# Kernel tuning notes

Measured on AMD Instinct MI355X. Metric: run time of the kernel, lower is better.

## Reference

```python
import jax, jax.numpy as jnp
import numpy as np

PI = float(np.pi)


def _layernorm(x, g, b, eps=1e-5):
    mu = jnp.mean(x, axis=-1, keepdims=True)
    var = jnp.var(x, axis=-1, keepdims=True)
    return (x - mu) * jax.lax.rsqrt(var + eps) * g + b


def setup_inputs() -> dict:
    key = jax.random.key(0)
    B, L, D, P = 4, 2048, 256, 32
    ks = jax.random.split(key, 16)

    def lin_w(k, fi, fo):
        return (jax.random.normal(k, (fi, fo), dtype=jnp.float32) / np.sqrt(fi)).astype(jnp.float32)

    inp = {
        'x': jax.random.normal(ks[0], (B, L, D), dtype=jnp.float32),
        'pos_phases': jax.random.normal(ks[1], (L, P), dtype=jnp.float32) * PI,
        'w_mem1v': lin_w(ks[2], D, P), 'b_mem1v': jnp.zeros((P,), jnp.float32),
        'w_mem1o': lin_w(ks[3], P, D), 'b_mem1o': jnp.zeros((D,), jnp.float32),
        'w_off': lin_w(ks[4], D + P, P), 'b_off': jnp.zeros((P,), jnp.float32),
        'w_key': lin_w(ks[5], D, P), 'b_key': jnp.zeros((P,), jnp.float32),
        'w_val': lin_w(ks[6], D, D), 'b_val': jnp.zeros((D,), jnp.float32),
        'w_sk1': lin_w(ks[7], 2 * D, D), 'b_sk1': jnp.zeros((D,), jnp.float32),
        'w_sk2': lin_w(ks[8], D, P), 'b_sk2': jnp.zeros((P,), jnp.float32),
        'w_gate': lin_w(ks[9], D, 1), 'b_gate': jnp.zeros((1,), jnp.float32),
        'ln_g': jnp.ones((D,), jnp.float32), 'ln_b': jnp.zeros((D,), jnp.float32),
        'w_out': lin_w(ks[10], D, D), 'b_out': jnp.zeros((D,), jnp.float32),
    }
    return inp


def reference(x, pos_phases, w_mem1v, b_mem1v, w_mem1o, b_mem1o, w_off, b_off,
              w_key, b_key, w_val, b_val, w_sk1, b_sk1, w_sk2, b_sk2,
              w_gate, b_gate, ln_g, ln_b, w_out, b_out):
    B, L, D = x.shape
    P = pos_phases.shape[-1]

    pos_cos = jnp.cos(pos_phases)  # [L,P]
    pos_sin = jnp.sin(pos_phases)

    # Memory 1: flat [B,L,P] phasor cumulative memory
    v1 = x @ w_mem1v + b_mem1v                       # [B,L,P]
    mem1_cos = jnp.cumsum(pos_cos[None] * v1, axis=1)
    mem1_sin = jnp.cumsum(pos_sin[None] * v1, axis=1)

    offset_input = jnp.concatenate([x, jnp.broadcast_to(pos_phases[None], (B, L, P))], axis=-1)
    offset = jnp.tanh(offset_input @ w_off + b_off) * PI
    oc, os = jnp.cos(offset), jnp.sin(offset)
    query_cos = pos_cos[None] * oc - pos_sin[None] * os
    query_sin = pos_sin[None] * oc + pos_cos[None] * os
    pos_ret = (mem1_cos * query_cos + mem1_sin * query_sin) / np.sqrt(P)
    pos_out = pos_ret @ w_mem1o + b_mem1o            # [B,L,D]

    # Memory 2: full [B,L,P,D] phasor KV cumulative memory
    key_phases = jnp.tanh(x @ w_key + b_key) * PI    # [B,L,P]
    key_cos, key_sin = jnp.cos(key_phases), jnp.sin(key_phases)
    values = x @ w_val + b_val                       # [B,L,D]
    store_gate = jax.nn.sigmoid(x @ w_gate + b_gate) # [B,L,1]

    positions = jnp.arange(1, L + 1, dtype=x.dtype)[None, :, None]
    context_avg = jnp.cumsum(x, axis=1) / positions
    h = jax.nn.gelu(jnp.concatenate([x, context_avg], axis=-1) @ w_sk1 + b_sk1, approximate=False)
    storage_phases = jnp.tanh(h @ w_sk2 + b_sk2) * PI  # [B,L,P]

    gated_v = values * store_gate                    # [B,L,D]
    kv_mem_cos = jnp.cumsum(jnp.cos(storage_phases)[..., None] * gated_v[:, :, None, :], axis=1)  # [B,L,P,D]
    kv_mem_sin = jnp.cumsum(jnp.sin(storage_phases)[..., None] * gated_v[:, :, None, :], axis=1)

    gate_cumsum = jnp.clip(jnp.cumsum(store_gate, axis=1), 1.0, None)  # [B,L,1]
    kv_retrieved = jnp.einsum('blpd,blp->bld', kv_mem_cos, key_cos) + \
                   jnp.einsum('blpd,blp->bld', kv_mem_sin, key_sin)
    kv_retrieved = kv_retrieved / (jnp.sqrt(gate_cumsum) * np.sqrt(P))

    combined = pos_out + kv_retrieved
    return x + _layernorm(combined, ln_g, ln_b) @ w_out + b_out
```

## Files before the change

kernel.cpp:

```cpp
#include <hip/hip_runtime.h>
#include <hip/hip_bf16.h>

constexpr int B_ = 4;
constexpr int L_ = 2048;
constexpr int D_ = 256;
constexpr int P_ = 32;
constexpr int CL = 32;
constexpr int NC = L_ / CL;

#define PI_F 3.14159265358979323846f
#define INV_SQRT_P 0.17677669529663687f

typedef __attribute__((ext_vector_type(8))) short short8_t;
typedef __attribute__((ext_vector_type(4))) float floatx4;

static __device__ inline short f2bf(float f) {
  unsigned int u;
  __builtin_memcpy(&u, &f, 4);
  unsigned int r = (u + 0x7fffu + ((u >> 16) & 1u)) >> 16;
  return (short)r;
}
static __device__ inline float bf2f(short s) {
  unsigned int u = ((unsigned int)(unsigned short)s) << 16;
  float f;
  __builtin_memcpy(&f, &u, 4);
  return f;
}

__global__ void wprep(const float* __restrict__ x, const float* __restrict__ pos,
                      const float* __restrict__ w_val, const float* __restrict__ w_mem1v,
                      const float* __restrict__ w_off, const float* __restrict__ b_off,
                      const float* __restrict__ w_key, const float* __restrict__ w_gate,
                      const float* __restrict__ w_sk1, const float* __restrict__ w_out,
                      const float* __restrict__ w_sk2, const float* __restrict__ w_mem1o,
                      short* __restrict__ WA, short* __restrict__ W1,
                      short* __restrict__ WO, short* __restrict__ W2T,
                      short* __restrict__ W1OT,
                      short* __restrict__ xbf, float* __restrict__ poff,
                      float* __restrict__ ctxsum) {
  int blk = blockIdx.x, tid = threadIdx.x;
  if (blk < 384) {
    int idx = blk * 256 + tid;
    int n = idx >> 8, k = idx & 255;
    float v;
    if (n < 256) v = w_val[k * 256 + n];
    else if (n < 288) v = w_mem1v[k * 32 + (n - 256)];
    else if (n < 320) v = w_off[k * 32 + (n - 288)];
    else if (n < 352) v = w_key[k * 32 + (n - 320)];
    else if (n == 352) v = w_gate[k];
    else v = 0.f;
    WA[idx] = f2bf(v);
  } else if (blk < 896) {
    int idx = (blk - 384) * 256 + tid;
    int n = idx >> 9, k = idx & 511;
    W1[idx] = f2bf(w_sk1[k * 256 + n]);
  } else if (blk < 1152) {
    int idx = (blk - 896) * 256 + tid;
    int n = idx >> 8, k = idx & 255;
    WO[idx] = f2bf(w_out[k * 256 + n]);
  } else if (blk < 1184) {
    int idx = (blk - 1152) * 256 + tid;
    int p = idx >> 8, k = idx & 255;
    W2T[idx] = f2bf(w_sk2[k * 32 + p]);
  } else if (blk < 1216) {
    int idx = (blk - 1184) * 256 + tid;
    int d = idx >> 5, p = idx & 31;
    W1OT[idx] = f2bf(w_mem1o[p * 256 + d]);
  } else if (blk < 3264) {
    int idx = ((blk - 1216) * 256 + tid) * 4;
    float4 v = *(const float4*)&x[idx];
    short4 o;
    o.x = f2bf(v.x); o.y = f2bf(v.y); o.z = f2bf(v.z); o.w = f2bf(v.w);
    *(short4*)&xbf[idx] = o;
  } else if (blk < 3520) {
    int idx = (blk - 3264) * 256 + tid;
    int l = idx >> 5, p = idx & 31;
    float a = b_off[p];
#pragma unroll 8
    for (int j = 0; j < 32; ++j) a += pos[l * 32 + j] * w_off[(256 + j) * 32 + p];
    poff[idx] = a;
  } else {
    int c2 = blk - 3520;
    int b = c2 >> 6, ch = c2 & 63;
    int xb = (b * L_ + ch * 32) * 256 + tid;
    float s = 0.f;
#pragma unroll 8
    for (int i = 0; i < 32; ++i) s += x[xb + i * 256];
    ctxsum[c2 * 256 + tid] = s;
  }
}

template <int KTILES, int MODE>
__global__ __launch_bounds__(256, 4) void gemm32(const short* __restrict__ A0,
                                                 const short* __restrict__ A1,
                                                 const short* __restrict__ W,
                                                 const float* __restrict__ bias,
                                                 const float* __restrict__ xres,
                                                 float* __restrict__ outf,
                                                 short* __restrict__ outb) {
  __shared__ short As[32][136];
  __shared__ short Bs[64][136];
  int tid = threadIdx.x;
  int mg = blockIdx.x >> 2, ng = blockIdx.x & 3;
  int tok0 = mg * 32, n0 = ng * 64;
  int lane = tid & 63, w = tid >> 6;
  int nw = w * 16;
  floatx4 acc[2] = {{0.f, 0.f, 0.f, 0.f}, {0.f, 0.f, 0.f, 0.f}};
  int r2 = tid >> 4, c8 = tid & 15;
  int ml = lane & 15, quad = lane >> 4, kq = quad * 8;
  const int K = KTILES * 128;

  for (int kt = 0; kt < KTILES; ++kt) {
    const short* Asrc;
    int cb;
    if (KTILES == 4) {
      Asrc = (kt < 2) ? A0 : A1;
      cb = (kt & 1) * 128;
    } else {
      Asrc = A0;
      cb = kt * 128;
    }
#pragma unroll
    for (int pass = 0; pass < 2; ++pass) {
      int row = pass * 16 + r2;
      *(short8_t*)&As[row][c8 * 8] =
          *(const short8_t*)&Asrc[(tok0 + row) * 256 + cb + c8 * 8];
    }
#pragma unroll
    for (int pass = 0; pass < 4; ++pass) {
      int row = pass * 16 + r2;
      *(short8_t*)&Bs[row][c8 * 8] =
          *(const short8_t*)&W[(n0 + row) * K + kt * 128 + c8 * 8];
    }
    __syncthreads();
#pragma unroll
    for (int s = 0; s < 4; ++s) {
      short8_t a0 = *(short8_t*)&As[ml][s * 32 + kq];
      short8_t a1 = *(short8_t*)&As[16 + ml][s * 32 + kq];
      short8_t b0 = *(short8_t*)&Bs[nw + ml][s * 32 + kq];
      acc[0] = __builtin_amdgcn_mfma_f32_16x16x32_bf16(a0, b0, acc[0], 0, 0, 0);
      acc[1] = __builtin_amdgcn_mfma_f32_16x16x32_bf16(a1, b0, acc[1], 0, 0, 0);
    }
    __syncthreads();
  }
  int n = n0 + nw + ml;
  float bv = bias ? bias[n] : 0.f;
#pragma unroll
  for (int mt = 0; mt < 2; ++mt) {
#pragma unroll
    for (int rg = 0; rg < 4; ++rg) {
      int tok = tok0 + mt * 16 + quad * 4 + rg;
      float v = acc[mt][rg] + bv;
      if (MODE == 1) {
        float g = 0.5f * v * (1.f + erff(v * 0.70710678118654752f));
        outb[tok * 256 + n] = f2bf(g);
      } else {
        outf[tok * 256 + n] = xres[tok * 256 + n] + v;
      }
    }
  }
}

__global__ __launch_bounds__(384, 3) void gemmA3(const short* __restrict__ xbf,
                                                 const short* __restrict__ WA,
                                                 const float* __restrict__ pos,
                                                 const float* __restrict__ poff,
                                                 const float* __restrict__ b_mem1v,
                                                 const float* __restrict__ b_key,
                                                 const float* __restrict__ b_gate,
                                                 const float* __restrict__ b_val,
                                                 float* __restrict__ m1cT,
                                                 float* __restrict__ m1sT,
                                                 float* __restrict__ qc,
                                                 float* __restrict__ qs,
                                                 short* __restrict__ K2bf,
                                                 short* __restrict__ gvT,
                                                 float* __restrict__ sg) {
  __shared__ float YL[16][132];
  __shared__ float gsh[16];
  int tid = threadIdx.x;
  int lane = tid & 63, w = tid >> 6;
  int ml = lane & 15, quad = lane >> 4, kq = quad * 8;
  int bc = blockIdx.x;
  int bc32 = bc >> 1, half = bc & 1;
  int tok0 = bc * 16;
  floatx4 acc[4] = {};
  const short* A0p = &xbf[(tok0 + ml) * 256 + kq];
  const short* Bp = &WA[(w * 64 + ml) * 256 + kq];
#pragma unroll
  for (int ks = 0; ks < 8; ++ks) {
    short8_t a0 = *(const short8_t*)(A0p + ks * 32);
#pragma unroll
    for (int nt = 0; nt < 4; ++nt) {
      short8_t b = *(const short8_t*)(Bp + nt * 16 * 256 + ks * 32);
      acc[nt] = __builtin_amdgcn_mfma_f32_16x16x32_bf16(a0, b, acc[nt], 0, 0, 0);
    }
  }
  if (w >= 4) {
#pragma unroll
    for (int nt = 0; nt < 4; ++nt) {
      int col = (w - 4) * 64 + nt * 16 + ml;
#pragma unroll
      for (int r = 0; r < 4; ++r)
        YL[quad * 4 + r][col] = acc[nt][r];
    }
  }
  __syncthreads();
  if (tid < 256) {
#pragma unroll
    for (int it = 0; it < 2; ++it) {
      int idx = it * 256 + tid;
      int t = idx >> 5, p = idx & 31;
      int tok = tok0 + t, l = tok & (L_ - 1);
      int b = tok >> 11;
      float v1 = YL[t][p] + b_mem1v[p];
      float ph = pos[l * 32 + p];
      float pc = cosf(ph), ps = sinf(ph);
      int idxT = (b * 32 + p) * L_ + l;
      m1cT[idxT] = pc * v1;
      m1sT[idxT] = ps * v1;
      float off = tanhf(YL[t][32 + p] + poff[l * 32 + p]) * PI_F;
      float oc = cosf(off), os = sinf(off);
      int gidx = tok * 32 + p;
      qc[gidx] = pc * oc - ps * os;
      qs[gidx] = ps * oc + pc * os;
      float kp = tanhf(YL[t][64 + p] + b_key[p]) * PI_F;
      K2bf[tok * 64 + p] = f2bf(cosf(kp));
      K2bf[tok * 64 + 32 + p] = f2bf(sinf(kp));
      if (p == 0) {
        float g = 1.f / (1.f + expf(-(YL[t][96] + b_gate[0])));
        sg[tok] = g;
        gsh[t] = g;
      }
    }
  }
  __syncthreads();
  if (w < 4) {
#pragma unroll
    for (int nt = 0; nt < 4; ++nt) {
      int d = w * 64 + nt * 16 + ml;
      float bv = b_val[d];
      int t0 = quad * 4;
      short4 o;
      o.x = f2bf((acc[nt][0] + bv) * gsh[t0 + 0]);
      o.y = f2bf((acc[nt][1] + bv) * gsh[t0 + 1]);
      o.z = f2bf((acc[nt][2] + bv) * gsh[t0 + 2]);
      o.w = f2bf((acc[nt][3] + bv) * gsh[t0 + 3]);
      *(short4*)&gvT[(bc32 * 256 + d) * 32 + half * 16 + t0] = o;
    }
  }
}

__global__ void scan_all(float* __restrict__ m1cT, float* __restrict__ m1sT,
                         float* __restrict__ sg, const float* __restrict__ x,
                         const float* __restrict__ ctxsum, short* __restrict__ ctxbf) {
  int blk = blockIdx.x;
  int tid = threadIdx.x;
  if (blk >= 260) {
    int c2 = blk - 260;
    int b = c2 >> 6, ch = c2 & 63;
    float run = 0.f;
    int sb = b * 64 * 256 + tid;
    int c = 0;
    for (; c + 8 <= ch; c += 8) {
      float t0 = ctxsum[sb + (c + 0) * 256];
      float t1 = ctxsum[sb + (c + 1) * 256];
      float t2 = ctxsum[sb + (c + 2) * 256];
      float t3 = ctxsum[sb + (c + 3) * 256];
      float t4 = ctxsum[sb + (c + 4) * 256];
      float t5 = ctxsum[sb + (c + 5) * 256];
      float t6 = ctxsum[sb + (c + 6) * 256];
      float t7 = ctxsum[sb + (c + 7) * 256];
      run += ((t0 + t1) + (t2 + t3)) + ((t4 + t5) + (t6 + t7));
    }
    for (; c < ch; ++c) run += ctxsum[sb + c * 256];
    int xb = (b * L_ + ch * 32) * 256 + tid;
#pragma unroll 8
    for (int i = 0; i < 32; ++i) {
      run += x[xb + i * 256];
      int l = ch * 32 + i;
      ctxbf[xb + i * 256] = f2bf(run / (float)(l + 1));
    }
    return;
  }
  int lane = tid & 63, wid = tid >> 6;
  __shared__ float wsum[4];
  float carry = 0.f;
  float* arr;
  int base;
  if (blk < 256) {
    arr = (blk < 128) ? m1cT : m1sT;
    base = (blk & 127) * L_;
  } else {
    arr = sg;
    base = (blk - 256) * L_;
  }
  float v[8];
#pragma unroll
  for (int i = 0; i < 8; ++i) v[i] = arr[base + i * 256 + tid];
#pragma unroll
  for (int i = 0; i < 8; ++i) {
    float vv = v[i];
#pragma unroll
    for (int off = 1; off < 64; off <<= 1) {
      float n = __shfl_up(vv, off, 64);
      if (lane >= off) vv += n;
    }
    if (lane == 63) wsum[wid] = vv;
    __syncthreads();
    float add = carry;
    for (int w = 0; w < wid; ++w) add += wsum[w];
    arr[base + i * 256 + tid] = vv + add;
    carry += wsum[0] + wsum[1] + wsum[2] + wsum[3];
    __syncthreads();
  }
}

__global__ __launch_bounds__(256, 2) void kernelCD(const short* __restrict__ hs,
                                                   const short* __restrict__ W2T,
                                                   const float* __restrict__ b_sk2,
                                                   const short* __restrict__ gvT,
                                                   short* __restrict__ SPbf,
                                                   short* __restrict__ UT) {
  __shared__ __align__(16) short SPL[64][40];
  int tid = threadIdx.x;
  int bc = blockIdx.x >> 1, dh = blockIdx.x & 1;
  int tok0 = bc * 32;
  int lane = tid & 63, w = tid >> 6;
  int ml = lane & 15, quad = lane >> 4, kq = quad * 8;
  int th = w & 1, ph = w >> 1;
  floatx4 pacc = {};
#pragma unroll
  for (int s = 0; s < 8; ++s) {
    short8_t a = *(const short8_t*)&hs[(tok0 + th * 16 + ml) * 256 + s * 32 + kq];
    short8_t b0 = *(const short8_t*)&W2T[(ph * 16 + ml) * 256 + s * 32 + kq];
    pacc = __builtin_amdgcn_mfma_f32_16x16x32_bf16(a, b0, pacc, 0, 0, 0);
  }
  {
    int p = ph * 16 + ml;
    float bs = b_sk2[p];
#pragma unroll
    for (int r = 0; r < 4; ++r) {
      int tl = th * 16 + quad * 4 + r;
      int tok = tok0 + tl;
      float sp = tanhf(pacc[r] + bs) * PI_F;
      short c = f2bf(cosf(sp)), s = f2bf(sinf(sp));
      SPL[p][tl] = c;
      SPL[32 + p][tl] = s;
      if (dh == 0) {
        SPbf[tok * 64 + p] = c;
        SPbf[tok * 64 + 32 + p] = s;
      }
    }
  }
  __syncthreads();
  short8_t a[4];
#pragma unroll
  for (int mt = 0; mt < 4; ++mt) a[mt] = *(short8_t*)&SPL[mt * 16 + ml][kq];
  floatx4 acc[4][2] = {};
#pragma unroll
  for (int nt = 0; nt < 2; ++nt) {
    int d = dh * 128 + w * 32 + nt * 16 + ml;
    short8_t b = *(const short8_t*)&gvT[(bc * 256 + d) * 32 + kq];
#pragma unroll
    for (int mt = 0; mt < 4; ++mt)
      acc[mt][nt] = __builtin_amdgcn_mfma_f32_16x16x32_bf16(a[mt], b, acc[mt][nt], 0, 0, 0);
  }
#pragma unroll
  for (int mt = 0; mt < 4; ++mt)
#pragma unroll
    for (int nt = 0; nt < 2; ++nt) {
      int d = dh * 128 + w * 32 + nt * 16 + ml;
      short4 o;
      o.x = f2bf(acc[mt][nt][0]);
      o.y = f2bf(acc[mt][nt][1]);
      o.z = f2bf(acc[mt][nt][2]);
      o.w = f2bf(acc[mt][nt][3]);
      *(short4*)&UT[(bc * 256 + d) * 64 + mt * 16 + quad * 4] = o;
    }
}

__global__ void kernelE(short* __restrict__ UT) {
  int tid = blockIdx.x * 256 + threadIdx.x;
  int q = tid & 63;
  int d = (tid >> 6) & 255;
  int b = tid >> 14;
  int base = ((b * NC) * 256 + d) * 64 + q;
  const int cs = 256 * 64;
  short v[64];
#pragma unroll
  for (int c = 0; c < 64; ++c) v[c] = UT[base + c * cs];
  float run = 0.f;
#pragma unroll
  for (int c = 0; c < 64; ++c) {
    UT[base + c * cs] = f2bf(run);
    run += bf2f(v[c]);
  }
}

__global__ __launch_bounds__(512, 2) void kernelFG(const short* __restrict__ UT,
                                                   const short* __restrict__ SPbf,
                                                   const short* __restrict__ K2bf,
                                                   const short* __restrict__ gvT,
                                                   const float* __restrict__ sgc,
                                                   const float* __restrict__ m1cT,
                                                   const float* __restrict__ m1sT,
                                                   const float* __restrict__ qc,
                                                   const float* __restrict__ qs,
                                                   const short* __restrict__ W1OT,
                                                   const float* __restrict__ b_mem1o,
                                                   const float* __restrict__ ln_g,
                                                   const float* __restrict__ ln_b,
                                                   short* __restrict__ cbn) {
  __shared__ __align__(16) short SL[32][40];
  __shared__ __align__(16) short PR[32][40];
  __shared__ float CMB[32][260];
  __shared__ float scl[32], mu_s[32], rs_s[32];
  int tid = threadIdx.x;
  int bc = blockIdx.x;
  int lbase = bc * CL;
  int bb = bc >> 6, lloc = (bc & 63) * 32;
  if (tid < 32) scl[tid] = rsqrtf(fmaxf(sgc[lbase + tid], 1.f)) * INV_SQRT_P;
#pragma unroll
  for (int it = 0; it < 2; ++it) {
    int i = it * 512 + tid;
    int p = i >> 5, t = i & 31;
    int gT = (bb * 32 + p) * L_ + lloc + t;
    int g = (lbase + t) * 32 + p;
    PR[t][p] = f2bf((m1cT[gT] * qc[g] + m1sT[gT] * qs[g]) * INV_SQRT_P);
  }
  int lane = tid & 63, w = tid >> 6;
  int ml = lane & 15, quad = lane >> 4, kq = quad * 8;
  int d0 = w * 32;
  floatx4 acc[2][2] = {};
  short8_t ka0 = *(const short8_t*)&K2bf[(lbase + ml) * 64 + kq];
  short8_t ka1 = *(const short8_t*)&K2bf[(lbase + 16 + ml) * 64 + kq];
  short8_t kb0 = *(const short8_t*)&K2bf[(lbase + ml) * 64 + 32 + kq];
  short8_t kb1 = *(const short8_t*)&K2bf[(lbase + 16 + ml) * 64 + 32 + kq];
#pragma unroll
  for (int nt = 0; nt < 2; ++nt) {
    short8_t b = *(const short8_t*)&UT[(bc * 256 + d0 + nt * 16 + ml) * 64 + kq];
    acc[0][nt] = __builtin_amdgcn_mfma_f32_16x16x32_bf16(ka0, b, acc[0][nt], 0, 0, 0);
    acc[1][nt] = __builtin_amdgcn_mfma_f32_16x16x32_bf16(ka1, b, acc[1][nt], 0, 0, 0);
  }
  if (w == 0) {
    floatx4 sacc[2][2] = {};
#pragma unroll
    for (int ks2 = 0; ks2 < 2; ++ks2) {
      short8_t a0 = (ks2 == 0) ? ka0 : kb0;
      short8_t a1 = (ks2 == 0) ? ka1 : kb1;
      short8_t b0 = *(const short8_t*)&SPbf[(lbase + ml) * 64 + ks2 * 32 + kq];
      short8_t b1 = *(const short8_t*)&SPbf[(lbase + 16 + ml) * 64 + ks2 * 32 + kq];
      sacc[0][0] = __builtin_amdgcn_mfma_f32_16x16x32_bf16(a0, b0, sacc[0][0], 0, 0, 0);
      sacc[0][1] = __builtin_amdgcn_mfma_f32_16x16x32_bf16(a0, b1, sacc[0][1], 0, 0, 0);
      sacc[1][0] = __builtin_amdgcn_mfma_f32_16x16x32_bf16(a1, b0, sacc[1][0], 0, 0, 0);
      sacc[1][1] = __builtin_amdgcn_mfma_f32_16x16x32_bf16(a1, b1, sacc[1][1], 0, 0, 0);
    }
#pragma unroll
    for (int mt = 0; mt < 2; ++mt)
#pragma unroll
      for (int nt = 0; nt < 2; ++nt)
#pragma unroll
        for (int r = 0; r < 4; ++r) {
          int trow = mt * 16 + quad * 4 + r;
          int scol = nt * 16 + ml;
          float v = (scol <= trow) ? sacc[mt][nt][r] : 0.f;
          SL[trow][scol] = f2bf(v);
        }
  }
  __syncthreads();
#pragma unroll
  for (int nt = 0; nt < 2; ++nt) {
    short8_t b = *(const short8_t*)&UT[(bc * 256 + d0 + nt * 16 + ml) * 64 + 32 + kq];
    acc[0][nt] = __builtin_amdgcn_mfma_f32_16x16x32_bf16(kb0, b, acc[0][nt], 0, 0, 0);
    acc[1][nt] = __builtin_amdgcn_mfma_f32_16x16x32_bf16(kb1, b, acc[1][nt], 0, 0, 0);
  }
  {
    short8_t a0 = *(short8_t*)&SL[ml][kq];
    short8_t a1 = *(short8_t*)&SL[16 + ml][kq];
#pragma unroll
    for (int nt = 0; nt < 2; ++nt) {
      short8_t b = *(const short8_t*)&gvT[(bc * 256 + d0 + nt * 16 + ml) * 32 + kq];
      acc[0][nt] = __builtin_amdgcn_mfma_f32_16x16x32_bf16(a0, b, acc[0][nt], 0, 0, 0);
      acc[1][nt] = __builtin_amdgcn_mfma_f32_16x16x32_bf16(a1, b, acc[1][nt], 0, 0, 0);
    }
  }
  floatx4 macc[2][2] = {};
  {
    short8_t a0 = *(short8_t*)&PR[ml][kq];
    short8_t a1 = *(short8_t*)&PR[16 + ml][kq];
#pragma unroll
    for (int nt = 0; nt < 2; ++nt) {
      short8_t b = *(const short8_t*)&W1OT[(d0 + nt * 16 + ml) * 32 + kq];
      macc[0][nt] = __builtin_amdgcn_mfma_f32_16x16x32_bf16(a0, b, macc[0][nt], 0, 0, 0);
      macc[1][nt] = __builtin_amdgcn_mfma_f32_16x16x32_bf16(a1, b, macc[1][nt], 0, 0, 0);
    }
  }
#pragma unroll
  for (int mt = 0; mt < 2; ++mt)
#pragma unroll
    for (int nt = 0; nt < 2; ++nt) {
      int d = d0 + nt * 16 + ml;
      float bm = b_mem1o[d];
#pragma unroll
      for (int r = 0; r < 4; ++r) {
        int t = mt * 16 + quad * 4 + r;
        CMB[t][d] = acc[mt][nt][r] * scl[t] + macc[mt][nt][r] + bm;
      }
    }
  __syncthreads();
  {
    int t = tid >> 4, g = tid & 15;
    float s = 0.f, s2 = 0.f;
#pragma unroll
    for (int j = 0; j < 16; ++j) {
      float v = CMB[t][g + j * 16];
      s += v;
      s2 += v * v;
    }
#pragma unroll
    for (int m = 1; m < 16; m <<= 1) {
      s += __shfl_xor(s, m, 64);
      s2 += __shfl_xor(s2, m, 64);
    }
    if (g == 0) {
      float mu = s / (float)D_;
      float var = s2 / (float)D_ - mu * mu;
      mu_s[t] = mu;
      rs_s[t] = rsqrtf(var + 1e-5f);
    }
  }
  __syncthreads();
  {
    int d = tid & 255, th = tid >> 8;
    float lg = ln_g[d], lb = ln_b[d];
#pragma unroll
    for (int i = 0; i < 16; ++i) {
      int t = th * 16 + i;
      cbn[(lbase + t) * 256 + d] = f2bf((CMB[t][d] - mu_s[t]) * rs_s[t] * lg + lb);
    }
  }
}

extern "C" void kernel_launch(void* const* d_in, const int* in_sizes, int n_in,
                              void* d_out, int out_size, void* d_ws, size_t ws_size,
                              hipStream_t stream) {
  const float* x = (const float*)d_in[0];
  const float* pos = (const float*)d_in[1];
  const float* w_mem1v = (const float*)d_in[2];
  const float* b_mem1v = (const float*)d_in[3];
  const float* w_mem1o = (const float*)d_in[4];
  const float* b_mem1o = (const float*)d_in[5];
  const float* w_off = (const float*)d_in[6];
  const float* b_off = (const float*)d_in[7];
  const float* w_key = (const float*)d_in[8];
  const float* b_key = (const float*)d_in[9];
  const float* w_val = (const float*)d_in[10];
  const float* b_val = (const float*)d_in[11];
  const float* w_sk1 = (const float*)d_in[12];
  const float* b_sk1 = (const float*)d_in[13];
  const float* w_sk2 = (const float*)d_in[14];
  const float* b_sk2 = (const float*)d_in[15];
  const float* w_gate = (const float*)d_in[16];
  const float* b_gate = (const float*)d_in[17];
  const float* ln_g = (const float*)d_in[18];
  const float* ln_b = (const float*)d_in[19];
  const float* w_out = (const float*)d_in[20];
  const float* b_out = (const float*)d_in[21];
  float* out = (float*)d_out;
  float* ws = (float*)d_ws;

  const int BLP = B_ * L_ * P_;
  const int BLD = B_ * L_ * D_;
  float* m1cT = ws;
  float* m1sT = m1cT + BLP;
  float* qc = m1sT + BLP;
  float* qs = qc + BLP;
  float* sg = qs + BLP;
  float* poff = sg + B_ * L_;
  float* ctxsum = poff + L_ * P_;
  short* UT = (short*)(ctxsum + B_ * 64 * 256);
  short* xbf = UT + (size_t)B_ * NC * 256 * 64;
  short* cbn = xbf;
  short* ctxbf = xbf + BLD;
  short* hs = ctxbf + BLD;
  short* gvT = hs + BLD;
  short* K2bf = gvT + BLD;
  short* SPbf = K2bf + B_ * L_ * 64;
  short* WA = SPbf + B_ * L_ * 64;
  short* W1 = WA + 384 * 256;
  short* WO = W1 + 256 * 512;
  short* W2T = WO + 256 * 256;
  short* W1OT = W2T + 32 * 256;

  wprep<<<3776, 256, 0, stream>>>(x, pos, w_val, w_mem1v, w_off, b_off, w_key, w_gate,
                                  w_sk1, w_out, w_sk2, w_mem1o, WA, W1, WO, W2T, W1OT,
                                  xbf, poff, ctxsum);
  gemmA3<<<512, 384, 0, stream>>>(xbf, WA, pos, poff, b_mem1v, b_key, b_gate, b_val,
                                  m1cT, m1sT, qc, qs, K2bf, gvT, sg);
  scan_all<<<516, 256, 0, stream>>>(m1cT, m1sT, sg, x, ctxsum, ctxbf);
  gemm32<4, 1><<<256 * 4, 256, 0, stream>>>(xbf, ctxbf, W1, b_sk1, nullptr, nullptr, hs);
  kernelCD<<<512, 256, 0, stream>>>(hs, W2T, b_sk2, gvT, SPbf, UT);
  kernelE<<<256, 256, 0, stream>>>(UT);
  kernelFG<<<B_ * NC, 512, 0, stream>>>(UT, SPbf, K2bf, gvT, sg, m1cT, m1sT, qc, qs,
                                        W1OT, b_mem1o, ln_g, ln_b, cbn);
  gemm32<2, 2><<<256 * 4, 256, 0, stream>>>(cbn, nullptr, WO, b_out, x, out, nullptr);
}
```

Before: 171.5 us.

## Merge all stages into one cooperative persistent kernel with grid syncs

```diff
diff --git a/kernel.cpp b/kernel.cpp
--- a/kernel.cpp
+++ b/kernel.cpp
@@ -1,5 +1,8 @@
 #include <hip/hip_runtime.h>
 #include <hip/hip_bf16.h>
+#include <hip/hip_cooperative_groups.h>
+
+namespace cg = cooperative_groups;
 
 constexpr int B_ = 4;
 constexpr int L_ = 2048;
@@ -27,519 +30,521 @@
   return f;
 }
 
-__global__ void wprep(const float* __restrict__ x, const float* __restrict__ pos,
-                      const float* __restrict__ w_val, const float* __restrict__ w_mem1v,
-                      const float* __restrict__ w_off, const float* __restrict__ b_off,
-                      const float* __restrict__ w_key, const float* __restrict__ w_gate,
-                      const float* __restrict__ w_sk1, const float* __restrict__ w_out,
-                      const float* __restrict__ w_sk2, const float* __restrict__ w_mem1o,
-                      short* __restrict__ WA, short* __restrict__ W1,
-                      short* __restrict__ WO, short* __restrict__ W2T,
-                      short* __restrict__ W1OT,
-                      short* __restrict__ xbf, float* __restrict__ poff,
-                      float* __restrict__ ctxsum) {
-  int blk = blockIdx.x, tid = threadIdx.x;
-  if (blk < 384) {
-    int idx = blk * 256 + tid;
-    int n = idx >> 8, k = idx & 255;
-    float v;
-    if (n < 256) v = w_val[k * 256 + n];
-    else if (n < 288) v = w_mem1v[k * 32 + (n - 256)];
-    else if (n < 320) v = w_off[k * 32 + (n - 288)];
-    else if (n < 352) v = w_key[k * 32 + (n - 320)];
-    else if (n == 352) v = w_gate[k];
-    else v = 0.f;
-    WA[idx] = f2bf(v);
-  } else if (blk < 896) {
-    int idx = (blk - 384) * 256 + tid;
-    int n = idx >> 9, k = idx & 511;
-    W1[idx] = f2bf(w_sk1[k * 256 + n]);
-  } else if (blk < 1152) {
-    int idx = (blk - 896) * 256 + tid;
-    int n = idx >> 8, k = idx & 255;
-    WO[idx] = f2bf(w_out[k * 256 + n]);
-  } else if (blk < 1184) {
-    int idx = (blk - 1152) * 256 + tid;
-    int p = idx >> 8, k = idx & 255;
-    W2T[idx] = f2bf(w_sk2[k * 32 + p]);
-  } else if (blk < 1216) {
-    int idx = (blk - 1184) * 256 + tid;
-    int d = idx >> 5, p = idx & 31;
-    W1OT[idx] = f2bf(w_mem1o[p * 256 + d]);
-  } else if (blk < 3264) {
-    int idx = ((blk - 1216) * 256 + tid) * 4;
-    float4 v = *(const float4*)&x[idx];
-    short4 o;
-    o.x = f2bf(v.x); o.y = f2bf(v.y); o.z = f2bf(v.z); o.w = f2bf(v.w);
-    *(short4*)&xbf[idx] = o;
-  } else if (blk < 3520) {
-    int idx = (blk - 3264) * 256 + tid;
-    int l = idx >> 5, p = idx & 31;
-    float a = b_off[p];
-#pragma unroll 8
-    for (int j = 0; j < 32; ++j) a += pos[l * 32 + j] * w_off[(256 + j) * 32 + p];
-    poff[idx] = a;
-  } else {
-    int c2 = blk - 3520;
-    int b = c2 >> 6, ch = c2 & 63;
-    int xb = (b * L_ + ch * 32) * 256 + tid;
-    float s = 0.f;
-#pragma unroll 8
-    for (int i = 0; i < 32; ++i) s += x[xb + i * 256];
-    ctxsum[c2 * 256 + tid] = s;
-  }
-}
+union __align__(16) SMem {
+  struct { float YL[2][16][132]; float gsh[2][16]; } a3;
+  struct { short As[2][32][136]; short Bs[2][64][136]; } g32;
+  struct { short SPL[2][64][40]; } cd;
+  struct { short SL[32][40]; short PR[32][40]; float CMB[32][260];
+           float scl[32]; float mu_s[32]; float rs_s[32]; } fg;
+};
 
 template <int KTILES, int MODE>
-__global__ __launch_bounds__(256, 4) void gemm32(const short* __restrict__ A0,
-                                                 const short* __restrict__ A1,
-                                                 const short* __restrict__ W,
-                                                 const float* __restrict__ bias,
-                                                 const float* __restrict__ xres,
-                                                 float* __restrict__ outf,
-                                                 short* __restrict__ outb) {
-  __shared__ short As[32][136];
-  __shared__ short Bs[64][136];
-  int tid = threadIdx.x;
-  int mg = blockIdx.x >> 2, ng = blockIdx.x & 3;
-  int tok0 = mg * 32, n0 = ng * 64;
+__device__ __forceinline__ void phase_gemm(const short* __restrict__ A0,
+                                           const short* __restrict__ A1,
+                                           const short* __restrict__ W,
+                                           const float* __restrict__ bias,
+                                           const float* __restrict__ xres,
+                                           float* __restrict__ outf,
+                                           short* __restrict__ outb,
+                                           SMem* sm, int bid, int tid5) {
+  int sub = tid5 >> 8, tid = tid5 & 255;
   int lane = tid & 63, w = tid >> 6;
   int nw = w * 16;
-  floatx4 acc[2] = {{0.f, 0.f, 0.f, 0.f}, {0.f, 0.f, 0.f, 0.f}};
   int r2 = tid >> 4, c8 = tid & 15;
   int ml = lane & 15, quad = lane >> 4, kq = quad * 8;
   const int K = KTILES * 128;
-
-  for (int kt = 0; kt < KTILES; ++kt) {
-    const short* Asrc;
-    int cb;
-    if (KTILES == 4) {
-      Asrc = (kt < 2) ? A0 : A1;
-      cb = (kt & 1) * 128;
+  for (int pass = 0; pass < 2; ++pass) {
+    int vb = pass * 512 + bid * 2 + sub;
+    int mg = vb >> 2, ng = vb & 3;
+    int tok0 = mg * 32, n0 = ng * 64;
+    floatx4 acc[2] = {{0.f, 0.f, 0.f, 0.f}, {0.f, 0.f, 0.f, 0.f}};
+    for (int kt = 0; kt < KTILES; ++kt) {
+      const short* Asrc;
+      int cb;
+      if (KTILES == 4) {
+        Asrc = (kt < 2) ? A0 : A1;
+        cb = (kt & 1) * 128;
+      } else {
+        Asrc = A0;
+        cb = kt * 128;
+      }
+#pragma unroll
+      for (int p2 = 0; p2 < 2; ++p2) {
+        int row = p2 * 16 + r2;
+        *(short8_t*)&sm->g32.As[sub][row][c8 * 8] =
+            *(const short8_t*)&Asrc[(tok0 + row) * 256 + cb + c8 * 8];
+      }
+#pragma unroll
+      for (int p2 = 0; p2 < 4; ++p2) {
+        int row = p2 * 16 + r2;
+        *(short8_t*)&sm->g32.Bs[sub][row][c8 * 8] =
+            *(const short8_t*)&W[(n0 + row) * K + kt * 128 + c8 * 8];
+      }
+      __syncthreads();
+#pragma unroll
+      for (int s = 0; s < 4; ++s) {
+        short8_t a0 = *(short8_t*)&sm->g32.As[sub][ml][s * 32 + kq];
+        short8_t a1 = *(short8_t*)&sm->g32.As[sub][16 + ml][s * 32 + kq];
+        short8_t b0 = *(short8_t*)&sm->g32.Bs[sub][nw + ml][s * 32 + kq];
+        acc[0] = __builtin_amdgcn_mfma_f32_16x16x32_bf16(a0, b0, acc[0], 0, 0, 0);
+        acc[1] = __builtin_amdgcn_mfma_f32_16x16x32_bf16(a1, b0, acc[1], 0, 0, 0);
+      }
+      __syncthreads();
+    }
+    int n = n0 + nw + ml;
+    float bv = bias[n];
+#pragma unroll
+    for (int mt = 0; mt < 2; ++mt) {
+#pragma unroll
+      for (int rg = 0; rg < 4; ++rg) {
+        int tok = tok0 + mt * 16 + quad * 4 + rg;
+        float v = acc[mt][rg] + bv;
+        if (MODE == 1) {
+          float g = 0.5f * v * (1.f + erff(v * 0.70710678118654752f));
+          outb[tok * 256 + n] = f2bf(g);
+        } else {
+          outf[tok * 256 + n] = xres[tok * 256 + n] + v;
+        }
+      }
+    }
+  }
+}
+
+__global__ __launch_bounds__(512, 2) void mega(
+    const float* __restrict__ x, const float* __restrict__ pos,
+    const float* __restrict__ w_val, const float* __restrict__ w_mem1v,
+    const float* __restrict__ w_off, const float* __restrict__ b_off,
+    const float* __restrict__ w_key, const float* __restrict__ w_gate,
+    const float* __restrict__ w_sk1, const float* __restrict__ w_out,
+    const float* __restrict__ w_sk2, const float* __restrict__ w_mem1o,
+    const float* __restrict__ b_mem1v, const float* __restrict__ b_key,
+    const float* __restrict__ b_gate, const float* __restrict__ b_val,
+    const float* __restrict__ b_sk1, const float* __restrict__ b_sk2,
+    const float* __restrict__ b_mem1o, const float* __restrict__ ln_g,
+    const float* __restrict__ ln_b, const float* __restrict__ b_out,
+    float* __restrict__ out, float* __restrict__ ws) {
+  __shared__ SMem sm;
+  cg::grid_group grid = cg::this_grid();
+  int bid = blockIdx.x;
+  int tid5 = threadIdx.x;
+  int sub = tid5 >> 8, tid = tid5 & 255;
+
+  const int BLP = B_ * L_ * P_;
+  const int BLD = B_ * L_ * D_;
+  float* m1cT = ws;
+  float* m1sT = m1cT + BLP;
+  float* qc = m1sT + BLP;
+  float* qs = qc + BLP;
+  float* sg = qs + BLP;
+  float* poff = sg + B_ * L_;
+  float* ctxsum = poff + L_ * P_;
+  short* UT = (short*)(ctxsum + B_ * 64 * 256);
+  short* xbf = UT + (size_t)B_ * NC * 256 * 64;
+  short* cbn = xbf;
+  short* ctxbf = xbf + BLD;
+  short* hs = ctxbf + BLD;
+  short* gvT = hs + BLD;
+  short* K2bf = gvT + BLD;
+  short* SPbf = K2bf + B_ * L_ * 64;
+  short* WA = SPbf + B_ * L_ * 64;
+  short* W1 = WA + 384 * 256;
+  short* WO = W1 + 256 * 512;
+  short* W2T = WO + 256 * 256;
+  short* W1OT = W2T + 32 * 256;
+
+  for (int p = 0; p < 8; ++p) {
+    int blk = p * 512 + bid * 2 + sub;
+    if (blk >= 3776) break;
+    if (blk < 384) {
+      int idx = blk * 256 + tid;
+      int n = idx >> 8, k = idx & 255;
+      float v;
+      if (n < 256) v = w_val[k * 256 + n];
+      else if (n < 288) v = w_mem1v[k * 32 + (n - 256)];
+      else if (n < 320) v = w_off[k * 32 + (n - 288)];
+      else if (n < 352) v = w_key[k * 32 + (n - 320)];
+      else if (n == 352) v = w_gate[k];
+      else v = 0.f;
+      WA[idx] = f2bf(v);
+    } else if (blk < 896) {
+      int idx = (blk - 384) * 256 + tid;
+      int n = idx >> 9, k = idx & 511;
+      W1[idx] = f2bf(w_sk1[k * 256 + n]);
+    } else if (blk < 1152) {
+      int idx = (blk - 896) * 256 + tid;
+      int n = idx >> 8, k = idx & 255;
+      WO[idx] = f2bf(w_out[k * 256 + n]);
+    } else if (blk < 1184) {
+      int idx = (blk - 1152) * 256 + tid;
+      int pp = idx >> 8, k = idx & 255;
+      W2T[idx] = f2bf(w_sk2[k * 32 + pp]);
+    } else if (blk < 1216) {
+      int idx = (blk - 1184) * 256 + tid;
+      int d = idx >> 5, pp = idx & 31;
+      W1OT[idx] = f2bf(w_mem1o[pp * 256 + d]);
+    } else if (blk < 3264) {
+      int idx = ((blk - 1216) * 256 + tid) * 4;
+      float4 v = *(const float4*)&x[idx];
+      short4 o;
+      o.x = f2bf(v.x); o.y = f2bf(v.y); o.z = f2bf(v.z); o.w = f2bf(v.w);
+      *(short4*)&xbf[idx] = o;
+    } else if (blk < 3520) {
+      int idx = (blk - 3264) * 256 + tid;
+      int l = idx >> 5, pp = idx & 31;
+      float a = b_off[pp];
+#pragma unroll 8
+      for (int j = 0; j < 32; ++j) a += pos[l * 32 + j] * w_off[(256 + j) * 32 + pp];
+      poff[idx] = a;
     } else {
-      Asrc = A0;
-      cb = kt * 128;
-    }
-#pragma unroll
-    for (int pass = 0; pass < 2; ++pass) {
-      int row = pass * 16 + r2;
-      *(short8_t*)&As[row][c8 * 8] =
-          *(const short8_t*)&Asrc[(tok0 + row) * 256 + cb + c8 * 8];
-    }
-#pragma unroll
-    for (int pass = 0; pass < 4; ++pass) {
-      int row = pass * 16 + r2;
-      *(short8_t*)&Bs[row][c8 * 8] =
-          *(const short8_t*)&W[(n0 + row) * K + kt * 128 + c8 * 8];
+      int c2 = blk - 3520;
+      int b = c2 >> 6, ch = c2 & 63;
+      int xb = (b * L_ + ch * 32) * 256 + tid;
+      float s = 0.f;
+#pragma unroll 8
+      for (int i = 0; i < 32; ++i) s += x[xb + i * 256];
+      ctxsum[c2 * 256 + tid] = s;
+    }
+  }
+  grid.sync();
+
+  {
+    int lane = tid & 63, w = tid >> 6;
+    int ml = lane & 15, quad = lane >> 4, kq = quad * 8;
+    int vb = bid * 2 + sub;
+    int bc32 = vb >> 1, half = vb & 1;
+    int tok0 = vb * 16;
+    floatx4 acc[6] = {};
+    const short* A0p = &xbf[(tok0 + ml) * 256 + kq];
+    const short* Bp = &WA[(w * 96 + ml) * 256 + kq];
+#pragma unroll
+    for (int ks = 0; ks < 8; ++ks) {
+      short8_t a0 = *(const short8_t*)(A0p + ks * 32);
+#pragma unroll
+      for (int nt = 0; nt < 6; ++nt) {
+        short8_t b = *(const short8_t*)(Bp + nt * 16 * 256 + ks * 32);
+        acc[nt] = __builtin_amdgcn_mfma_f32_16x16x32_bf16(a0, b, acc[nt], 0, 0, 0);
+      }
+    }
+#pragma unroll
+    for (int nt = 0; nt < 6; ++nt) {
+      int col = w * 96 + nt * 16 + ml;
+      if (col >= 256) {
+#pragma unroll
+        for (int r = 0; r < 4; ++r) sm.a3.YL[sub][quad * 4 + r][col - 256] = acc[nt][r];
+      }
     }
     __syncthreads();
-#pragma unroll
-    for (int s = 0; s < 4; ++s) {
-      short8_t a0 = *(short8_t*)&As[ml][s * 32 + kq];
-      short8_t a1 = *(short8_t*)&As[16 + ml][s * 32 + kq];
-      short8_t b0 = *(short8_t*)&Bs[nw + ml][s * 32 + kq];
-      acc[0] = __builtin_amdgcn_mfma_f32_16x16x32_bf16(a0, b0, acc[0], 0, 0, 0);
-      acc[1] = __builtin_amdgcn_mfma_f32_16x16x32_bf16(a1, b0, acc[1], 0, 0, 0);
-    }
-    __syncthreads();
-  }
-  int n = n0 + nw + ml;
-  float bv = bias ? bias[n] : 0.f;
-#pragma unroll
-  for (int mt = 0; mt < 2; ++mt) {
-#pragma unroll
-    for (int rg = 0; rg < 4; ++rg) {
-      int tok = tok0 + mt * 16 + quad * 4 + rg;
-      float v = acc[mt][rg] + bv;
-      if (MODE == 1) {
-        float g = 0.5f * v * (1.f + erff(v * 0.70710678118654752f));
-        outb[tok * 256 + n] = f2bf(g);
-      } else {
-        outf[tok * 256 + n] = xres[tok * 256 + n] + v;
-      }
-    }
-  }
-}
-
-__global__ __launch_bounds__(384, 3) void gemmA3(const short* __restrict__ xbf,
-                                                 const short* __restrict__ WA,
-                                                 const float* __restrict__ pos,
-                                                 const float* __restrict__ poff,
-                                                 const float* __restrict__ b_mem1v,
-                                                 const float* __restrict__ b_key,
-                                                 const float* __restrict__ b_gate,
-                                                 const float* __restrict__ b_val,
-                                                 float* __restrict__ m1cT,
-                                                 float* __restrict__ m1sT,
-                                                 float* __restrict__ qc,
-                                                 float* __restrict__ qs,
-                                                 short* __restrict__ K2bf,
-                                                 short* __restrict__ gvT,
-                                                 float* __restrict__ sg) {
-  __shared__ float YL[16][132];
-  __shared__ float gsh[16];
-  int tid = threadIdx.x;
-  int lane = tid & 63, w = tid >> 6;
-  int ml = lane & 15, quad = lane >> 4, kq = quad * 8;
-  int bc = blockIdx.x;
-  int bc32 = bc >> 1, half = bc & 1;
-  int tok0 = bc * 16;
-  floatx4 acc[4] = {};
-  const short* A0p = &xbf[(tok0 + ml) * 256 + kq];
-  const short* Bp = &WA[(w * 64 + ml) * 256 + kq];
-#pragma unroll
-  for (int ks = 0; ks < 8; ++ks) {
-    short8_t a0 = *(const short8_t*)(A0p + ks * 32);
-#pragma unroll
-    for (int nt = 0; nt < 4; ++nt) {
-      short8_t b = *(const short8_t*)(Bp + nt * 16 * 256 + ks * 32);
-      acc[nt] = __builtin_amdgcn_mfma_f32_16x16x32_bf16(a0, b, acc[nt], 0, 0, 0);
-    }
-  }
-  if (w >= 4) {
-#pragma unroll
-    for (int nt = 0; nt < 4; ++nt) {
-      int col = (w - 4) * 64 + nt * 16 + ml;
-#pragma unroll
-      for (int r = 0; r < 4; ++r)
-        YL[quad * 4 + r][col] = acc[nt][r];
-    }
-  }
-  __syncthreads();
-  if (tid < 256) {
 #pragma unroll
     for (int it = 0; it < 2; ++it) {
       int idx = it * 256 + tid;
-      int t = idx >> 5, p = idx & 31;
+      int t = idx >> 5, pp = idx & 31;
       int tok = tok0 + t, l = tok & (L_ - 1);
       int b = tok >> 11;
-      float v1 = YL[t][p] + b_mem1v[p];
-      float ph = pos[l * 32 + p];
+      float v1 = sm.a3.YL[sub][t][pp] + b_mem1v[pp];
+      float ph = pos[l * 32 + pp];
       float pc = cosf(ph), ps = sinf(ph);
-      int idxT = (b * 32 + p) * L_ + l;
+      int idxT = (b * 32 + pp) * L_ + l;
       m1cT[idxT] = pc * v1;
       m1sT[idxT] = ps * v1;
-      float off = tanhf(YL[t][32 + p] + poff[l * 32 + p]) * PI_F;
+      float off = tanhf(sm.a3.YL[sub][t][32 + pp] + poff[l * 32 + pp]) * PI_F;
       float oc = cosf(off), os = sinf(off);
-      int gidx = tok * 32 + p;
+      int gidx = tok * 32 + pp;
       qc[gidx] = pc * oc - ps * os;
       qs[gidx] = ps * oc + pc * os;
-      float kp = tanhf(YL[t][64 + p] + b_key[p]) * PI_F;
-      K2bf[tok * 64 + p] = f2bf(cosf(kp));
-      K2bf[tok * 64 + 32 + p] = f2bf(sinf(kp));
-      if (p == 0) {
-        float g = 1.f / (1.f + expf(-(YL[t][96] + b_gate[0])));
+      float kp = tanhf(sm.a3.YL[sub][t][64 + pp] + b_key[pp]) * PI_F;
+      K2bf[tok * 64 + pp] = f2bf(cosf(kp));
+      K2bf[tok * 64 + 32 + pp] = f2bf(sinf(kp));
+      if (pp == 0) {
+        float g = 1.f / (1.f + expf(-(sm.a3.YL[sub][t][96] + b_gate[0])));
         sg[tok] = g;
-        gsh[t] = g;
-      }
-    }
-  }
-  __syncthreads();
-  if (w < 4) {
-#pragma unroll
-    for (int nt = 0; nt < 4; ++nt) {
-      int d = w * 64 + nt * 16 + ml;
-      float bv = b_val[d];
-      int t0 = quad * 4;
-      short4 o;
-      o.x = f2bf((acc[nt][0] + bv) * gsh[t0 + 0]);
-      o.y = f2bf((acc[nt][1] + bv) * gsh[t0 + 1]);
-      o.z = f2bf((acc[nt][2] + bv) * gsh[t0 + 2]);
-      o.w = f2bf((acc[nt][3] + bv) * gsh[t0 + 3]);
-      *(short4*)&gvT[(bc32 * 256 + d) * 32 + half * 16 + t0] = o;
-    }
-  }
-}
-
-__global__ void scan_all(float* __restrict__ m1cT, float* __restrict__ m1sT,
-                         float* __restrict__ sg, const float* __restrict__ x,
-                         const float* __restrict__ ctxsum, short* __restrict__ ctxbf) {
-  int blk = blockIdx.x;
-  int tid = threadIdx.x;
-  if (blk >= 260) {
-    int c2 = blk - 260;
-    int b = c2 >> 6, ch = c2 & 63;
-    float run = 0.f;
-    int sb = b * 64 * 256 + tid;
-    int c = 0;
-    for (; c + 8 <= ch; c += 8) {
-      float t0 = ctxsum[sb + (c + 0) * 256];
-      float t1 = ctxsum[sb + (c + 1) * 256];
-      float t2 = ctxsum[sb + (c + 2) * 256];
-      float t3 = ctxsum[sb + (c + 3) * 256];
-      float t4 = ctxsum[sb + (c + 4) * 256];
-      float t5 = ctxsum[sb + (c + 5) * 256];
-      float t6 = ctxsum[sb + (c + 6) * 256];
-      float t7 = ctxsum[sb + (c + 7) * 256];
-      run += ((t0 + t1) + (t2 + t3)) + ((t4 + t5) + (t6 + t7));
-    }
-    for (; c < ch; ++c) run += ctxsum[sb + c * 256];
-    int xb = (b * L_ + ch * 32) * 256 + tid;
+        sm.a3.gsh[sub][t] = g;
+      }
+    }
+    __syncthreads();
+#pragma unroll
+    for (int nt = 0; nt < 6; ++nt) {
+      int col = w * 96 + nt * 16 + ml;
+      if (col < 256) {
+        float bv = b_val[col];
+        int t0 = quad * 4;
+        short4 o;
+        o.x = f2bf((acc[nt][0] + bv) * sm.a3.gsh[sub][t0 + 0]);
+        o.y = f2bf((acc[nt][1] + bv) * sm.a3.gsh[sub][t0 + 1]);
+        o.z = f2bf((acc[nt][2] + bv) * sm.a3.gsh[sub][t0 + 2]);
+        o.w = f2bf((acc[nt][3] + bv) * sm.a3.gsh[sub][t0 + 3]);
+        *(short4*)&gvT[(bc32 * 256 + col) * 32 + half * 16 + t0] = o;
+      }
+    }
+  }
+  grid.sync();
+
+  {
+    int gw = bid * 8 + (tid5 >> 6);
+    int lane = tid5 & 63;
+    if (gw < 260) {
+      float* arr;
+      int base;
+      if (gw < 128) { arr = m1cT; base = gw * L_; }
+      else if (gw < 256) { arr = m1sT; base = (gw - 128) * L_; }
+      else { arr = sg; base = (gw - 256) * L_; }
+      float v[32];
+#pragma unroll
+      for (int i = 0; i < 32; ++i) v[i] = arr[base + i * 64 + lane];
+      float carry = 0.f;
+#pragma unroll
+      for (int i = 0; i < 32; ++i) {
+        float vv = v[i];
+#pragma unroll
+        for (int off = 1; off < 64; off <<= 1) {
+          float n = __shfl_up(vv, off, 64);
+          if (lane >= off) vv += n;
+        }
+        vv += carry;
+        arr[base + i * 64 + lane] = vv;
+        carry = __shfl(vv, 63, 64);
+      }
+    } else if (gw >= 1024) {
+      int ct = gw - 1024;
+      int c2 = ct >> 2, dp = ct & 3;
+      int b = c2 >> 6, ch = c2 & 63;
+      int d = dp * 64 + lane;
+      float run = 0.f;
+      int sb = b * 64 * 256 + d;
+      int c = 0;
+      for (; c + 8 <= ch; c += 8) {
+        float t0 = ctxsum[sb + (c + 0) * 256];
+        float t1 = ctxsum[sb + (c + 1) * 256];
+        float t2 = ctxsum[sb + (c + 2) * 256];
+        float t3 = ctxsum[sb + (c + 3) * 256];
+        float t4 = ctxsum[sb + (c + 4) * 256];
+        float t5 = ctxsum[sb + (c + 5) * 256];
+        float t6 = ctxsum[sb + (c + 6) * 256];
+        float t7 = ctxsum[sb + (c + 7) * 256];
+        run += ((t0 + t1) + (t2 + t3)) + ((t4 + t5) + (t6 + t7));
+      }
+      for (; c < ch; ++c) run += ctxsum[sb + c * 256];
+      int xb = (b * L_ + ch * 32) * 256 + d;
 #pragma unroll 8
-    for (int i = 0; i < 32; ++i) {
-      run += x[xb + i * 256];
-      int l = ch * 32 + i;
-      ctxbf[xb + i * 256] = f2bf(run / (float)(l + 1));
-    }
-    return;
-  }
-  int lane = tid & 63, wid = tid >> 6;
-  __shared__ float wsum[4];
-  float carry = 0.f;
-  float* arr;
-  int base;
-  if (blk < 256) {
-    arr = (blk < 128) ? m1cT : m1sT;
-    base = (blk & 127) * L_;
-  } else {
-    arr = sg;
-    base = (blk - 256) * L_;
-  }
-  float v[8];
-#pragma unroll
-  for (int i = 0; i < 8; ++i) v[i] = arr[base + i * 256 + tid];
-#pragma unroll
-  for (int i = 0; i < 8; ++i) {
-    float vv = v[i];
-#pragma unroll
-    for (int off = 1; off < 64; off <<= 1) {
-      float n = __shfl_up(vv, off, 64);
-      if (lane >= off) vv += n;
-    }
-    if (lane == 63) wsum[wid] = vv;
+      for (int i = 0; i < 32; ++i) {
+        run += x[xb + i * 256];
+        int l = ch * 32 + i;
+        ctxbf[xb + i * 256] = f2bf(run / (float)(l + 1));
+      }
+    }
+  }
+  grid.sync();
+
+  phase_gemm<4, 1>(xbf, ctxbf, W1, b_sk1, nullptr, nullptr, hs, &sm, bid, tid5);
+  grid.sync();
+
+  {
+    int lane = tid & 63, w = tid >> 6;
+    int ml = lane & 15, quad = lane >> 4, kq = quad * 8;
+    int vb = bid * 2 + sub;
+    int bc = vb >> 1, dh = vb & 1;
+    int tok0 = bc * 32;
+    int th = w & 1, ph = w >> 1;
+    floatx4 pacc = {};
+#pragma unroll
+    for (int s = 0; s < 8; ++s) {
+      short8_t a = *(const short8_t*)&hs[(tok0 + th * 16 + ml) * 256 + s * 32 + kq];
+      short8_t b0 = *(const short8_t*)&W2T[(ph * 16 + ml) * 256 + s * 32 + kq];
+      pacc = __builtin_amdgcn_mfma_f32_16x16x32_bf16(a, b0, pacc, 0, 0, 0);
+    }
+    {
+      int pp = ph * 16 + ml;
+      float bs = b_sk2[pp];
+#pragma unroll
+      for (int r = 0; r < 4; ++r) {
+        int tl = th * 16 + quad * 4 + r;
+        int tok = tok0 + tl;
+        float sp = tanhf(pacc[r] + bs) * PI_F;
+        short c = f2bf(cosf(sp)), s2 = f2bf(sinf(sp));
+        sm.cd.SPL[sub][pp][tl] = c;
+        sm.cd.SPL[sub][32 + pp][tl] = s2;
+        if (dh == 0) {
+          SPbf[tok * 64 + pp] = c;
+          SPbf[tok * 64 + 32 + pp] = s2;
+        }
+      }
+    }
     __syncthreads();
-    float add = carry;
-    for (int w = 0; w < wid; ++w) add += wsum[w];
-    arr[base + i * 256 + tid] = vv + add;
-    carry += wsum[0] + wsum[1] + wsum[2] + wsum[3];
-    __syncthreads();
-  }
-}
-
-__global__ __launch_bounds__(256, 2) void kernelCD(const short* __restrict__ hs,
-                                                   const short* __restrict__ W2T,
-                                                   const float* __restrict__ b_sk2,
-                                                   const short* __restrict__ gvT,
-                                                   short* __restrict__ SPbf,
-                                                   short* __restrict__ UT) {
-  __shared__ __align__(16) short SPL[64][40];
-  int tid = threadIdx.x;
-  int bc = blockIdx.x >> 1, dh = blockIdx.x & 1;
-  int tok0 = bc * 32;
-  int lane = tid & 63, w = tid >> 6;
-  int ml = lane & 15, quad = lane >> 4, kq = quad * 8;
-  int th = w & 1, ph = w >> 1;
-  floatx4 pacc = {};
-#pragma unroll
-  for (int s = 0; s < 8; ++s) {
-    short8_t a = *(const short8_t*)&hs[(tok0 + th * 16 + ml) * 256 + s * 32 + kq];
-    short8_t b0 = *(const short8_t*)&W2T[(ph * 16 + ml) * 256 + s * 32 + kq];
-    pacc = __builtin_amdgcn_mfma_f32_16x16x32_bf16(a, b0, pacc, 0, 0, 0);
-  }
-  {
-    int p = ph * 16 + ml;
-    float bs = b_sk2[p];
-#pragma unroll
-    for (int r = 0; r < 4; ++r) {
-      int tl = th * 16 + quad * 4 + r;
-      int tok = tok0 + tl;
-      float sp = tanhf(pacc[r] + bs) * PI_F;
-      short c = f2bf(cosf(sp)), s = f2bf(sinf(sp));
-      SPL[p][tl] = c;
-      SPL[32 + p][tl] = s;
-      if (dh == 0) {
-        SPbf[tok * 64 + p] = c;
-        SPbf[tok * 64 + 32 + p] = s;
-      }
-    }
-  }
-  __syncthreads();
-  short8_t a[4];
-#pragma unroll
-  for (int mt = 0; mt < 4; ++mt) a[mt] = *(short8_t*)&SPL[mt * 16 + ml][kq];
-  floatx4 acc[4][2] = {};
-#pragma unroll
-  for (int nt = 0; nt < 2; ++nt) {
-    int d = dh * 128 + w * 32 + nt * 16 + ml;
-    short8_t b = *(const short8_t*)&gvT[(bc * 256 + d) * 32 + kq];
-#pragma unroll
-    for (int mt = 0; mt < 4; ++mt)
-      acc[mt][nt] = __builtin_amdgcn_mfma_f32_16x16x32_bf16(a[mt], b, acc[mt][nt], 0, 0, 0);
-  }
-#pragma unroll
-  for (int mt = 0; mt < 4; ++mt)
+    short8_t a[4];
+#pragma unroll
+    for (int mt = 0; mt < 4; ++mt) a[mt] = *(short8_t*)&sm.cd.SPL[sub][mt * 16 + ml][kq];
+    floatx4 acc[4][2] = {};
 #pragma unroll
     for (int nt = 0; nt < 2; ++nt) {
       int d = dh * 128 + w * 32 + nt * 16 + ml;
-      short4 o;
-      o.x = f2bf(acc[mt][nt][0]);
-      o.y = f2bf(acc[mt][nt][1]);
-      o.z = f2bf(acc[mt][nt][2]);
-      o.w = f2bf(acc[mt][nt][3]);
-      *(short4*)&UT[(bc * 256 + d) * 64 + mt * 16 + quad * 4] = o;
-    }
-}
-
-__global__ void kernelE(short* __restrict__ UT) {
-  int tid = blockIdx.x * 256 + threadIdx.x;
-  int q = tid & 63;
-  int d = (tid >> 6) & 255;
-  int b = tid >> 14;
-  int base = ((b * NC) * 256 + d) * 64 + q;
-  const int cs = 256 * 64;
-  short v[64];
-#pragma unroll
-  for (int c = 0; c < 64; ++c) v[c] = UT[base + c * cs];
-  float run = 0.f;
-#pragma unroll
-  for (int c = 0; c < 64; ++c) {
-    UT[base + c * cs] = f2bf(run);
-    run += bf2f(v[c]);
-  }
-}
-
-__global__ __launch_bounds__(512, 2) void kernelFG(const short* __restrict__ UT,
-                                                   const short* __restrict__ SPbf,
-                                                   const short* __restrict__ K2bf,
-                                                   const short* __restrict__ gvT,
-                                                   const float* __restrict__ sgc,
-                                                   const float* __restrict__ m1cT,
-                                                   const float* __restrict__ m1sT,
-                                                   const float* __restrict__ qc,
-                                                   const float* __restrict__ qs,
-                                                   const short* __restrict__ W1OT,
-                                                   const float* __restrict__ b_mem1o,
-                                                   const float* __restrict__ ln_g,
-                                                   const float* __restrict__ ln_b,
-                                                   short* __restrict__ cbn) {
-  __shared__ __align__(16) short SL[32][40];
-  __shared__ __align__(16) short PR[32][40];
-  __shared__ float CMB[32][260];
-  __shared__ float scl[32], mu_s[32], rs_s[32];
-  int tid = threadIdx.x;
-  int bc = blockIdx.x;
-  int lbase = bc * CL;
-  int bb = bc >> 6, lloc = (bc & 63) * 32;
-  if (tid < 32) scl[tid] = rsqrtf(fmaxf(sgc[lbase + tid], 1.f)) * INV_SQRT_P;
-#pragma unroll
-  for (int it = 0; it < 2; ++it) {
-    int i = it * 512 + tid;
-    int p = i >> 5, t = i & 31;
-    int gT = (bb * 32 + p) * L_ + lloc + t;
-    int g = (lbase + t) * 32 + p;
-    PR[t][p] = f2bf((m1cT[gT] * qc[g] + m1sT[gT] * qs[g]) * INV_SQRT_P);
-  }
-  int lane = tid & 63, w = tid >> 6;
-  int ml = lane & 15, quad = lane >> 4, kq = quad * 8;
-  int d0 = w * 32;
-  floatx4 acc[2][2] = {};
-  short8_t ka0 = *(const short8_t*)&K2bf[(lbase + ml) * 64 + kq];
-  short8_t ka1 = *(const short8_t*)&K2bf[(lbase + 16 + ml) * 64 + kq];
-  short8_t kb0 = *(const short8_t*)&K2bf[(lbase + ml) * 64 + 32 + kq];
-  short8_t kb1 = *(const short8_t*)&K2bf[(lbase + 16 + ml) * 64 + 32 + kq];
-#pragma unroll
-  for (int nt = 0; nt < 2; ++nt) {
-    short8_t b = *(const short8_t*)&UT[(bc * 256 + d0 + nt * 16 + ml) * 64 + kq];
-    acc[0][nt] = __builtin_amdgcn_mfma_f32_16x16x32_bf16(ka0, b, acc[0][nt], 0, 0, 0);
-    acc[1][nt] = __builtin_amdgcn_mfma_f32_16x16x32_bf16(ka1, b, acc[1][nt], 0, 0, 0);
-  }
-  if (w == 0) {
-    floatx4 sacc[2][2] = {};
-#pragma unroll
-    for (int ks2 = 0; ks2 < 2; ++ks2) {
-      short8_t a0 = (ks2 == 0) ? ka0 : kb0;
-      short8_t a1 = (ks2 == 0) ? ka1 : kb1;
-      short8_t b0 = *(const short8_t*)&SPbf[(lbase + ml) * 64 + ks2 * 32 + kq];
-      short8_t b1 = *(const short8_t*)&SPbf[(lbase + 16 + ml) * 64 + ks2 * 32 + kq];
-      sacc[0][0] = __builtin_amdgcn_mfma_f32_16x16x32_bf16(a0, b0, sacc[0][0], 0, 0, 0);
-      sacc[0][1] = __builtin_amdgcn_mfma_f32_16x16x32_bf16(a0, b1, sacc[0][1], 0, 0, 0);
-      sacc[1][0] = __builtin_amdgcn_mfma_f32_16x16x32_bf16(a1, b0, sacc[1][0], 0, 0, 0);
-      sacc[1][1] = __builtin_amdgcn_mfma_f32_16x16x32_bf16(a1, b1, sacc[1][1], 0, 0, 0);
+      short8_t b = *(const short8_t*)&gvT[(bc * 256 + d) * 32 + kq];
+#pragma unroll
+      for (int mt = 0; mt < 4; ++mt)
+        acc[mt][nt] = __builtin_amdgcn_mfma_f32_16x16x32_bf16(a[mt], b, acc[mt][nt], 0, 0, 0);
+    }
+#pragma unroll
+    for (int mt = 0; mt < 4; ++mt)
+#pragma unroll
+      for (int nt = 0; nt < 2; ++nt) {
+        int d = dh * 128 + w * 32 + nt * 16 + ml;
+        short4 o;
+        o.x = f2bf(acc[mt][nt][0]);
+        o.y = f2bf(acc[mt][nt][1]);
+        o.z = f2bf(acc[mt][nt][2]);
+        o.w = f2bf(acc[mt][nt][3]);
+        *(short4*)&UT[(bc * 256 + d) * 64 + mt * 16 + quad * 4] = o;
+      }
+  }
+  grid.sync();
+
+  {
+    int vt = bid * 512 + tid5;
+    if (vt < 65536) {
+      int q = vt & 63;
+      int d = (vt >> 6) & 255;
+      int b = vt >> 14;
+      int base = ((b * NC) * 256 + d) * 64 + q;
+      const int cs = 256 * 64;
+      short v[64];
+#pragma unroll
+      for (int c = 0; c < 64; ++c) v[c] = UT[base + c * cs];
+      float run = 0.f;
+#pragma unroll
+      for (int c = 0; c < 64; ++c) {
+        UT[base + c * cs] = f2bf(run);
+        run += bf2f(v[c]);
+      }
+    }
+  }
+  grid.sync();
+
+  {
+    int bc = bid;
+    int lbase = bc * CL;
+    int bb = bc >> 6, lloc = (bc & 63) * 32;
+    if (tid5 < 32) sm.fg.scl[tid5] = rsqrtf(fmaxf(sg[lbase + tid5], 1.f)) * INV_SQRT_P;
+#pragma unroll
+    for (int it = 0; it < 2; ++it) {
+      int i = it * 512 + tid5;
+      int pp = i >> 5, t = i & 31;
+      int gT = (bb * 32 + pp) * L_ + lloc + t;
+      int g = (lbase + t) * 32 + pp;
+      sm.fg.PR[t][pp] = f2bf((m1cT[gT] * qc[g] + m1sT[gT] * qs[g]) * INV_SQRT_P);
+    }
+    int lane = tid5 & 63, w = tid5 >> 6;
+    int ml = lane & 15, quad = lane >> 4, kq = quad * 8;
+    int d0 = w * 32;
+    floatx4 acc[2][2] = {};
+    short8_t ka0 = *(const short8_t*)&K2bf[(lbase + ml) * 64 + kq];
+    short8_t ka1 = *(const short8_t*)&K2bf[(lbase + 16 + ml) * 64 + kq];
+    short8_t kb0 = *(const short8_t*)&K2bf[(lbase + ml) * 64 + 32 + kq];
+    short8_t kb1 = *(const short8_t*)&K2bf[(lbase + 16 + ml) * 64 + 32 + kq];
+#pragma unroll
+    for (int nt = 0; nt < 2; ++nt) {
+      short8_t b = *(const short8_t*)&UT[(bc * 256 + d0 + nt * 16 + ml) * 64 + kq];
+      acc[0][nt] = __builtin_amdgcn_mfma_f32_16x16x32_bf16(ka0, b, acc[0][nt], 0, 0, 0);
+      acc[1][nt] = __builtin_amdgcn_mfma_f32_16x16x32_bf16(ka1, b, acc[1][nt], 0, 0, 0);
+    }
+    if (w == 0) {
+      floatx4 sacc[2][2] = {};
+#pragma unroll
+      for (int ks2 = 0; ks2 < 2; ++ks2) {
+        short8_t a0 = (ks2 == 0) ? ka0 : kb0;
+        short8_t a1 = (ks2 == 0) ? ka1 : kb1;
+        short8_t b0 = *(const short8_t*)&SPbf[(lbase + ml) * 64 + ks2 * 32 + kq];
+        short8_t b1 = *(const short8_t*)&SPbf[(lbase + 16 + ml) * 64 + ks2 * 32 + kq];
+        sacc[0][0] = __builtin_amdgcn_mfma_f32_16x16x32_bf16(a0, b0, sacc[0][0], 0, 0, 0);
+        sacc[0][1] = __builtin_amdgcn_mfma_f32_16x16x32_bf16(a0, b1, sacc[0][1], 0, 0, 0);
+        sacc[1][0] = __builtin_amdgcn_mfma_f32_16x16x32_bf16(a1, b0, sacc[1][0], 0, 0, 0);
+        sacc[1][1] = __builtin_amdgcn_mfma_f32_16x16x32_bf16(a1, b1, sacc[1][1], 0, 0, 0);
+      }
+#pragma unroll
+      for (int mt = 0; mt < 2; ++mt)
+#pragma unroll
+        for (int nt = 0; nt < 2; ++nt)
+#pragma unroll
+          for (int r = 0; r < 4; ++r) {
+            int trow = mt * 16 + quad * 4 + r;
+            int scol = nt * 16 + ml;
+            float v = (scol <= trow) ? sacc[mt][nt][r] : 0.f;
+            sm.fg.SL[trow][scol] = f2bf(v);
+          }
+    }
+    __syncthreads();
+#pragma unroll
+    for (int nt = 0; nt < 2; ++nt) {
+      short8_t b = *(const short8_t*)&UT[(bc * 256 + d0 + nt * 16 + ml) * 64 + 32 + kq];
+      acc[0][nt] = __builtin_amdgcn_mfma_f32_16x16x32_bf16(kb0, b, acc[0][nt], 0, 0, 0);
+      acc[1][nt] = __builtin_amdgcn_mfma_f32_16x16x32_bf16(kb1, b, acc[1][nt], 0, 0, 0);
+    }
+    {
+      short8_t a0 = *(short8_t*)&sm.fg.SL[ml][kq];
+      short8_t a1 = *(short8_t*)&sm.fg.SL[16 + ml][kq];
+#pragma unroll
+      for (int nt = 0; nt < 2; ++nt) {
+        short8_t b = *(const short8_t*)&gvT[(bc * 256 + d0 + nt * 16 + ml) * 32 + kq];
+        acc[0][nt] = __builtin_amdgcn_mfma_f32_16x16x32_bf16(a0, b, acc[0][nt], 0, 0, 0);
+        acc[1][nt] = __builtin_amdgcn_mfma_f32_16x16x32_bf16(a1, b, acc[1][nt], 0, 0, 0);
+      }
+    }
+    floatx4 macc[2][2] = {};
+    {
+      short8_t a0 = *(short8_t*)&sm.fg.PR[ml][kq];
+      short8_t a1 = *(short8_t*)&sm.fg.PR[16 + ml][kq];
+#pragma unroll
+      for (int nt = 0; nt < 2; ++nt) {
+        short8_t b = *(const short8_t*)&W1OT[(d0 + nt * 16 + ml) * 32 + kq];
+        macc[0][nt] = __builtin_amdgcn_mfma_f32_16x16x32_bf16(a0, b, macc[0][nt], 0, 0, 0);
+        macc[1][nt] = __builtin_amdgcn_mfma_f32_16x16x32_bf16(a1, b, macc[1][nt], 0, 0, 0);
+      }
     }
 #pragma unroll
     for (int mt = 0; mt < 2; ++mt)
 #pragma unroll
-      for (int nt = 0; nt < 2; ++nt)
+      for (int nt = 0; nt < 2; ++nt) {
+        int d = d0 + nt * 16 + ml;
+        float bm = b_mem1o[d];
 #pragma unroll
         for (int r = 0; r < 4; ++r) {
-          int trow = mt * 16 + quad * 4 + r;
-          int scol = nt * 16 + ml;
-          float v = (scol <= trow) ? sacc[mt][nt][r] : 0.f;
-          SL[trow][scol] = f2bf(v);
+          int t = mt * 16 + quad * 4 + r;
+          sm.fg.CMB[t][d] = acc[mt][nt][r] * sm.fg.scl[t] + macc[mt][nt][r] + bm;
         }
-  }
-  __syncthreads();
-#pragma unroll
-  for (int nt = 0; nt < 2; ++nt) {
-    short8_t b = *(const short8_t*)&UT[(bc * 256 + d0 + nt * 16 + ml) * 64 + 32 + kq];
-    acc[0][nt] = __builtin_amdgcn_mfma_f32_16x16x32_bf16(kb0, b, acc[0][nt], 0, 0, 0);
-    acc[1][nt] = __builtin_amdgcn_mfma_f32_16x16x32_bf16(kb1, b, acc[1][nt], 0, 0, 0);
-  }
-  {
-    short8_t a0 = *(short8_t*)&SL[ml][kq];
-    short8_t a1 = *(short8_t*)&SL[16 + ml][kq];
-#pragma unroll
-    for (int nt = 0; nt < 2; ++nt) {
-      short8_t b = *(const short8_t*)&gvT[(bc * 256 + d0 + nt * 16 + ml) * 32 + kq];
-      acc[0][nt] = __builtin_amdgcn_mfma_f32_16x16x32_bf16(a0, b, acc[0][nt], 0, 0, 0);
-      acc[1][nt] = __builtin_amdgcn_mfma_f32_16x16x32_bf16(a1, b, acc[1][nt], 0, 0, 0);
-    }
-  }
-  floatx4 macc[2][2] = {};
-  {
-    short8_t a0 = *(short8_t*)&PR[ml][kq];
-    short8_t a1 = *(short8_t*)&PR[16 + ml][kq];
-#pragma unroll
-    for (int nt = 0; nt < 2; ++nt) {
-      short8_t b = *(const short8_t*)&W1OT[(d0 + nt * 16 + ml) * 32 + kq];
-      macc[0][nt] = __builtin_amdgcn_mfma_f32_16x16x32_bf16(a0, b, macc[0][nt], 0, 0, 0);
-      macc[1][nt] = __builtin_amdgcn_mfma_f32_16x16x32_bf16(a1, b, macc[1][nt], 0, 0, 0);
-    }
-  }
-#pragma unroll
-  for (int mt = 0; mt < 2; ++mt)
-#pragma unroll
-    for (int nt = 0; nt < 2; ++nt) {
-      int d = d0 + nt * 16 + ml;
-      float bm = b_mem1o[d];
-#pragma unroll
-      for (int r = 0; r < 4; ++r) {
-        int t = mt * 16 + quad * 4 + r;
-        CMB[t][d] = acc[mt][nt][r] * scl[t] + macc[mt][nt][r] + bm;
-      }
-    }
-  __syncthreads();
-  {
-    int t = tid >> 4, g = tid & 15;
-    float s = 0.f, s2 = 0.f;
-#pragma unroll
-    for (int j = 0; j < 16; ++j) {
-      float v = CMB[t][g + j * 16];
-      s += v;
-      s2 += v * v;
-    }
-#pragma unroll
-    for (int m = 1; m < 16; m <<= 1) {
-      s += __shfl_xor(s, m, 64);
-      s2 += __shfl_xor(s2, m, 64);
-    }
-    if (g == 0) {
-      float mu = s / (float)D_;
-      float var = s2 / (float)D_ - mu * mu;
-      mu_s[t] = mu;
-      rs_s[t] = rsqrtf(var + 1e-5f);
-    }
-  }
-  __syncthreads();
-  {
-    int d = tid & 255, th = tid >> 8;
-    float lg = ln_g[d], lb = ln_b[d];
-#pragma unroll
-    for (int i = 0; i < 16; ++i) {
-      int t = th * 16 + i;
-      cbn[(lbase + t) * 256 + d] = f2bf((CMB[t][d] - mu_s[t]) * rs_s[t] * lg + lb);
-    }
-  }
+      }
+    __syncthreads();
+    {
+      int t = tid5 >> 4, g = tid5 & 15;
+      float s = 0.f, s2 = 0.f;
+#pragma unroll
+      for (int j = 0; j < 16; ++j) {
+        float v = sm.fg.CMB[t][g + j * 16];
+        s += v;
+        s2 += v * v;
+      }
+#pragma unroll
+      for (int m = 1; m < 16; m <<= 1) {
+        s += __shfl_xor(s, m, 64);
+        s2 += __shfl_xor(s2, m, 64);
+      }
+      if (g == 0) {
+        float mu = s / (float)D_;
+        float var = s2 / (float)D_ - mu * mu;
+        sm.fg.mu_s[t] = mu;
+        sm.fg.rs_s[t] = rsqrtf(var + 1e-5f);
+      }
+    }
+    __syncthreads();
+    {
+      int d = tid5 & 255, th = tid5 >> 8;
+      float lg = ln_g[d], lb = ln_b[d];
+#pragma unroll
+      for (int i = 0; i < 16; ++i) {
+        int t = th * 16 + i;
+        cbn[(lbase + t) * 256 + d] = f2bf((sm.fg.CMB[t][d] - sm.fg.mu_s[t]) * sm.fg.rs_s[t] * lg + lb);
+      }
+    }
+  }
+  grid.sync();
+
+  phase_gemm<2, 2>(cbn, nullptr, WO, b_out, x, out, nullptr, &sm, bid, tid5);
 }
 
 extern "C" void kernel_launch(void* const* d_in, const int* in_sizes, int n_in,
@@ -570,39 +575,12 @@
   float* out = (float*)d_out;
   float* ws = (float*)d_ws;
 
-  const int BLP = B_ * L_ * P_;
-  const int BLD = B_ * L_ * D_;
-  float* m1cT = ws;
-  float* m1sT = m1cT + BLP;
-  float* qc = m1sT + BLP;
-  float* qs = qc + BLP;
-  float* sg = qs + BLP;
-  float* poff = sg + B_ * L_;
-  float* ctxsum = poff + L_ * P_;
-  short* UT = (short*)(ctxsum + B_ * 64 * 256);
-  short* xbf = UT + (size_t)B_ * NC * 256 * 64;
-  short* cbn = xbf;
-  short* ctxbf = xbf + BLD;
-  short* hs = ctxbf + BLD;
-  short* gvT = hs + BLD;
-  short* K2bf = gvT + BLD;
-  short* SPbf = K2bf + B_ * L_ * 64;
-  short* WA = SPbf + B_ * L_ * 64;
-  short* W1 = WA + 384 * 256;
-  short* WO = W1 + 256 * 512;
-  short* W2T = WO + 256 * 256;
-  short* W1OT = W2T + 32 * 256;
-
-  wprep<<<3776, 256, 0, stream>>>(x, pos, w_val, w_mem1v, w_off, b_off, w_key, w_gate,
-                                  w_sk1, w_out, w_sk2, w_mem1o, WA, W1, WO, W2T, W1OT,
-                                  xbf, poff, ctxsum);
-  gemmA3<<<512, 384, 0, stream>>>(xbf, WA, pos, poff, b_mem1v, b_key, b_gate, b_val,
-                                  m1cT, m1sT, qc, qs, K2bf, gvT, sg);
-  scan_all<<<516, 256, 0, stream>>>(m1cT, m1sT, sg, x, ctxsum, ctxbf);
-  gemm32<4, 1><<<256 * 4, 256, 0, stream>>>(xbf, ctxbf, W1, b_sk1, nullptr, nullptr, hs);
-  kernelCD<<<512, 256, 0, stream>>>(hs, W2T, b_sk2, gvT, SPbf, UT);
-  kernelE<<<256, 256, 0, stream>>>(UT);
-  kernelFG<<<B_ * NC, 512, 0, stream>>>(UT, SPbf, K2bf, gvT, sg, m1cT, m1sT, qc, qs,
-                                        W1OT, b_mem1o, ln_g, ln_b, cbn);
-  gemm32<2, 2><<<256 * 4, 256, 0, stream>>>(cbn, nullptr, WO, b_out, x, out, nullptr);
+  void* args[] = {
+      (void*)&x, (void*)&pos, (void*)&w_val, (void*)&w_mem1v,
+      (void*)&w_off, (void*)&b_off, (void*)&w_key, (void*)&w_gate,
+      (void*)&w_sk1, (void*)&w_out, (void*)&w_sk2, (void*)&w_mem1o,
+      (void*)&b_mem1v, (void*)&b_key, (void*)&b_gate, (void*)&b_val,
+      (void*)&b_sk1, (void*)&b_sk2, (void*)&b_mem1o, (void*)&ln_g,
+      (void*)&ln_b, (void*)&b_out, (void*)&out, (void*)&ws};
+  hipLaunchCooperativeKernel((const void*)mega, dim3(256), dim3(512), args, 0, stream);
 }
```

New measurement: 413.2 us. +141.0%, slower.
